# Kernel optimization log

Hardware: AMD Instinct MI355X
Metric: run time of the kernel (lower is better)

The kernel has to match this reference:

```python
import jax, jax.numpy as jnp
import numpy as np


def _causal_conv(x, w, b, dilation):
    # x: (B, Cin, N), w: (Cout, Cin, K) -> causal: left-pad (K-1)*dilation
    pad = (w.shape[-1] - 1) * dilation
    y = jax.lax.conv_general_dilated(
        x, w, window_strides=(1,), padding=[(pad, 0)],
        rhs_dilation=(dilation,), dimension_numbers=('NCH', 'OIH', 'NCH'))
    return y + b[None, :, None]


def setup_inputs() -> dict:
    key = jax.random.key(0)
    ks = jax.random.split(key, 8)
    B, N, C, L = 8, 32768, 16, 30
    s = 0.1  # weight scale to avoid gate saturation
    return {
        'x': jax.random.normal(ks[0], (B, N), dtype=jnp.float32) * 1000.0,  # int16-like samples
        'lengths': jax.random.randint(ks[1], (B,), N // 2, N),
        'w0': jax.random.normal(ks[2], (C, 1, 2), dtype=jnp.float32) * s,
        'b0': jnp.zeros((C,), jnp.float32),
        'wf': jax.random.normal(ks[3], (L - 1, C, C, 2), dtype=jnp.float32) * s,
        'bf': jnp.zeros((L - 1, C), jnp.float32),
        'wg': jax.random.normal(ks[4], (L - 1, C, C, 2), dtype=jnp.float32) * s,
        'bg': jnp.zeros((L - 1, C), jnp.float32),
        'wa': jax.random.normal(ks[5], (64, C), dtype=jnp.float32) * s,
        'ba': jnp.zeros((64,), jnp.float32),
        'wo': jax.random.normal(ks[6], (256, 64), dtype=jnp.float32) * s,
        'bo': jnp.zeros((256,), jnp.float32),
    }


def reference(x, lengths, w0, b0, wf, bf, wg, bg, wa, ba, wo, bo):
    L = wf.shape[0] + 1  # total layers (layer 0 is plain causal conv)
    xin = (x / 32768.0)[:, None, :]            # (B,1,N), int16 normalization 65536/2
    out0 = _causal_conv(xin, w0, b0, 1)        # (B,C,N)
    agg = out0                                 # skip aggregate
    h = xin + out0                             # residual input (broadcast 1->C channels)
    for i in range(1, L):                      # fixed small layer count
        d = 2 ** (i % 10)
        f = _causal_conv(h, wf[i - 1], bf[i - 1], d)
        g = _causal_conv(h, wg[i - 1], bg[i - 1], d)
        out = jnp.tanh(f) * jax.nn.sigmoid(g)  # gated activation unit
        agg = agg + out
        h = h + out
    a = jnp.einsum('oc,bcn->bon', wa, jax.nn.relu(agg)) + ba[None, :, None]  # agregate1x1
    o = jnp.einsum('oc,bcn->bon', wo, jax.nn.relu(a)) + bo[None, :, None]    # output1x1
    o = jax.nn.log_softmax(o, axis=1)
    mask = (jnp.arange(o.shape[-1]) < lengths[:, None]).astype(o.dtype)      # (B,N)
    return o * mask[:, None, :]
```

## Files before the change

### kernel.cpp

```cpp
#include <hip/hip_runtime.h>

#define NSEQ 32768
#define NB 8
#define NC 16
#define LBLK 1024
#define LPX (LBLK / 8)
#define QGRD 4096
#define QPX (QGRD / 8)

typedef float vfloat4 __attribute__((ext_vector_type(4)));

__device__ __forceinline__ float sigm_f(float x) {
    return __fdividef(1.f, 1.f + __expf(-x));
}
__device__ __forceinline__ float tanh_f(float x) {
    return __fdividef(2.f, 1.f + __expf(-2.f * x)) - 1.f;
}

__device__ __forceinline__ void nt_store4(float* p, float a, float b, float c, float d) {
    vfloat4 v; v.x = a; v.y = b; v.z = c; v.w = d;
    __builtin_nontemporal_store(v, (vfloat4*)p);
}

__global__ __launch_bounds__(256) void k_layer0(
    const float* __restrict__ x, const float* __restrict__ w0,
    const float* __restrict__ b0, float* __restrict__ h)
{
    int bid = blockIdx.x;
    int tid = ((bid & 7) * LPX + (bid >> 3)) * 256 + threadIdx.x;
    int n = tid & (NSEQ - 1);
    const float inv = 1.f / 32768.f;
    float xc = x[tid] * inv;
    float xp = (n >= 1) ? x[tid - 1] * inv : 0.f;
    float v[NC];
#pragma unroll
    for (int c = 0; c < NC; c++) {
        float o = w0[c * 2] * xp + w0[c * 2 + 1] * xc + b0[c];
        v[c] = xc + o;
    }
    float* ph = h + (size_t)tid * NC;
#pragma unroll
    for (int i = 0; i < 4; i++)
        nt_store4(ph + i * 4, v[i * 4], v[i * 4 + 1], v[i * 4 + 2], v[i * 4 + 3]);
}

__global__ __launch_bounds__(256, 6) void k_layer(
    const float* __restrict__ hin, float* __restrict__ hout,
    const float* __restrict__ wf, const float* __restrict__ bf,
    const float* __restrict__ wg, const float* __restrict__ bg, int d)
{
    int bid = blockIdx.x;
    int lbid = (bid & 7) * QPX + (bid >> 3);
    int t = threadIdx.x;
    int pos = lbid * 64 + (t & 63);
    int q = __builtin_amdgcn_readfirstlane(t >> 6);
    int n = pos & (NSEQ - 1);

    float hc[NC], hp[NC];
    {
        const float4* pc = (const float4*)(hin + (size_t)pos * NC);
#pragma unroll
        for (int i = 0; i < 4; i++) {
            float4 tv = pc[i];
            hc[i * 4] = tv.x; hc[i * 4 + 1] = tv.y; hc[i * 4 + 2] = tv.z; hc[i * 4 + 3] = tv.w;
        }
    }
    if (n >= d) {
        const float4* pp = (const float4*)(hin + (size_t)(pos - d) * NC);
#pragma unroll
        for (int i = 0; i < 4; i++) {
            float4 tv = pp[i];
            hp[i * 4] = tv.x; hp[i * 4 + 1] = tv.y; hp[i * 4 + 2] = tv.z; hp[i * 4 + 3] = tv.w;
        }
    } else {
#pragma unroll
        for (int i = 0; i < NC; i++) hp[i] = 0.f;
    }

    const int c0 = q * 4;
    float f[4], g[4];
#pragma unroll
    for (int j = 0; j < 4; j++) { f[j] = bf[c0 + j]; g[j] = bg[c0 + j]; }

#pragma unroll
    for (int ci = 0; ci < NC; ci++) {
        float xp = hp[ci], xc = hc[ci];
#pragma unroll
        for (int j = 0; j < 4; j++) {
            int co = c0 + j;
            f[j] = fmaf(wf[(co * NC + ci) * 2 + 0], xp, f[j]);
            f[j] = fmaf(wf[(co * NC + ci) * 2 + 1], xc, f[j]);
            g[j] = fmaf(wg[(co * NC + ci) * 2 + 0], xp, g[j]);
            g[j] = fmaf(wg[(co * NC + ci) * 2 + 1], xc, g[j]);
        }
    }

    float v[4];
#pragma unroll
    for (int j = 0; j < 4; j++) {
        float outv = tanh_f(f[j]) * sigm_f(g[j]);
        v[j] = hc[c0 + j] + outv;
    }
    nt_store4(hout + (size_t)pos * NC + c0, v[0], v[1], v[2], v[3]);
}

__global__ __launch_bounds__(256) void k_prep_t(
    const float* __restrict__ wo, float* __restrict__ woT)
{
    int t = blockIdx.x * 256 + threadIdx.x;
    int k = t >> 6;
    int j = t & 63;
    woT[j * 256 + k] = wo[k * 64 + j];
}

__global__ __launch_bounds__(512, 4) void k_final(
    const float* __restrict__ hfin, const float* __restrict__ x,
    const int* __restrict__ lengths,
    const float* __restrict__ wa, const float* __restrict__ ba,
    const float* __restrict__ woT, const float* __restrict__ bo,
    float* __restrict__ out)
{
    __shared__ float s_r[64][17];
    __shared__ float s_ra[64][65];
    __shared__ float s_red[2][8][64];

    int t = threadIdx.x;
    int p = t & 63;
    int q = __builtin_amdgcn_readfirstlane(t >> 6);
    int blk = blockIdx.x;
    int b = blk >> 9;
    int n0 = (blk & 511) << 6;
    int n = n0 + p;
    size_t pos = (size_t)b * NSEQ + n;
    float xin = x[pos] * (1.f / 32768.f);

    if (q < 4) {
        const float4* ph = (const float4*)(hfin + pos * NC);
        float4 v = ph[q];
        s_r[p][q * 4 + 0] = fmaxf(v.x - xin, 0.f);
        s_r[p][q * 4 + 1] = fmaxf(v.y - xin, 0.f);
        s_r[p][q * 4 + 2] = fmaxf(v.z - xin, 0.f);
        s_r[p][q * 4 + 3] = fmaxf(v.w - xin, 0.f);
    }
    __syncthreads();

    {
        float r[NC];
#pragma unroll
        for (int c = 0; c < NC; c++) r[c] = s_r[p][c];
#pragma unroll
        for (int jj = 0; jj < 8; jj++) {
            int j = q * 8 + jj;
            float acc = ba[j];
#pragma unroll
            for (int c = 0; c < NC; c++) acc = fmaf(wa[j * NC + c], r[c], acc);
            s_ra[p][j] = fmaxf(acc, 0.f);
        }
    }
    __syncthreads();

    float o[32];
#pragma unroll
    for (int kk = 0; kk < 32; kk++) o[kk] = bo[q * 32 + kk];

#pragma unroll 8
    for (int j = 0; j < 64; j++) {
        float rj = s_ra[p][j];
        const float* wcol = woT + j * 256 + q * 32;
#pragma unroll
        for (int kk = 0; kk < 32; kk++)
            o[kk] = fmaf(wcol[kk], rj, o[kk]);
    }

    float m = -1e30f;
#pragma unroll
    for (int kk = 0; kk < 32; kk++) m = fmaxf(m, o[kk]);
    s_red[0][q][p] = m;
    __syncthreads();
    m = fmaxf(fmaxf(fmaxf(s_red[0][0][p], s_red[0][1][p]),
                    fmaxf(s_red[0][2][p], s_red[0][3][p])),
              fmaxf(fmaxf(s_red[0][4][p], s_red[0][5][p]),
                    fmaxf(s_red[0][6][p], s_red[0][7][p])));
    float s = 0.f;
#pragma unroll
    for (int kk = 0; kk < 32; kk++) s += __expf(o[kk] - m);
    s_red[1][q][p] = s;
    __syncthreads();
    s = ((s_red[1][0][p] + s_red[1][1][p]) + (s_red[1][2][p] + s_red[1][3][p]))
      + ((s_red[1][4][p] + s_red[1][5][p]) + (s_red[1][6][p] + s_red[1][7][p]));
    float lse = m + __logf(s);

    bool valid = n < lengths[b];
    float* po = out + ((size_t)b * 256 + q * 32) * NSEQ + n;
#pragma unroll
    for (int kk = 0; kk < 32; kk++) {
        float v = valid ? (o[kk] - lse) : 0.f;
        __builtin_nontemporal_store(v, &po[(size_t)kk * NSEQ]);
    }
}

extern "C" void kernel_launch(void* const* d_in, const int* in_sizes, int n_in,
                              void* d_out, int out_size, void* d_ws, size_t ws_size,
                              hipStream_t stream) {
    const float* x   = (const float*)d_in[0];
    const int* lens  = (const int*)d_in[1];
    const float* w0  = (const float*)d_in[2];
    const float* b0  = (const float*)d_in[3];
    const float* wf  = (const float*)d_in[4];
    const float* bf  = (const float*)d_in[5];
    const float* wg  = (const float*)d_in[6];
    const float* bg  = (const float*)d_in[7];
    const float* wa  = (const float*)d_in[8];
    const float* ba  = (const float*)d_in[9];
    const float* wo  = (const float*)d_in[10];
    const float* bo  = (const float*)d_in[11];
    float* out = (float*)d_out;

    float* hA = (float*)d_ws;
    float* hB = hA + (size_t)NB * NSEQ * NC;
    float* woT = hB + (size_t)NB * NSEQ * NC;

    k_prep_t<<<dim3(64), dim3(256), 0, stream>>>(wo, woT);
    k_layer0<<<dim3(LBLK), dim3(256), 0, stream>>>(x, w0, b0, hA);

    float* cur = hA;
    float* nxt = hB;
    for (int i = 1; i <= 29; i++) {
        int d = 1 << (i % 10);
        k_layer<<<dim3(QGRD), dim3(256), 0, stream>>>(cur, nxt,
                                         wf + (size_t)(i - 1) * NC * NC * 2,
                                         bf + (size_t)(i - 1) * NC,
                                         wg + (size_t)(i - 1) * NC * NC * 2,
                                         bg + (size_t)(i - 1) * NC, d);
        float* tmp = cur; cur = nxt; nxt = tmp;
    }

    dim3 fgrd(NB * (NSEQ / 64));
    k_final<<<fgrd, dim3(512), 0, stream>>>(cur, x, lens, wa, ba, woT, bo, out);
}
```

Baseline: 577.6 us.

## Fuse pairs of small-dilation layers into one kernel with LDS halo

Adds a k_pair kernel that computes two consecutive gated conv layers in one launch. The first layer's output for the 64-position tile, plus a halo of dB earlier positions, is recomputed and kept in shared memory, and the second layer then reads from it. Pairs are used where the second dilation is at most 16 (layers 1-4, 9-14, 19-24), so eight intermediate full-tensor writes and reads to global memory are removed. The cost is redundant computation of halo positions, an extra barrier, and lower occupancy from the shared-memory buffer and launch bounds.

```diff
diff --git a/kernel.cpp b/kernel.cpp
--- a/kernel.cpp
+++ b/kernel.cpp
@@ -102,6 +102,118 @@
         v[j] = hc[c0 + j] + outv;
     }
     nt_store4(hout + (size_t)pos * NC + c0, v[0], v[1], v[2], v[3]);
+}
+
+__global__ __launch_bounds__(256, 5) void k_pair(
+    const float* __restrict__ hin, float* __restrict__ hout,
+    const float* __restrict__ wfA, const float* __restrict__ bfA,
+    const float* __restrict__ wgA, const float* __restrict__ bgA, int dA,
+    const float* __restrict__ wfB, const float* __restrict__ bfB,
+    const float* __restrict__ wgB, const float* __restrict__ bgB, int dB)
+{
+    __shared__ float hsA[NC][80];
+    int bid = blockIdx.x;
+    int lbid = (bid & 7) * QPX + (bid >> 3);
+    int t = threadIdx.x;
+    int lane = t & 63;
+    int q = __builtin_amdgcn_readfirstlane(t >> 6);
+    const int c0 = q * 4;
+    int P = lbid * 64;
+    int n0 = P & (NSEQ - 1);
+
+#pragma unroll 1
+    for (int pass = 0; pass < 2; ++pass) {
+        int pos  = pass ? (P + lane) : (P - dB + lane);
+        int act  = pass ? 1 : ((lane < dB) && (n0 > 0));
+        int slot = pass ? (dB + lane) : lane;
+        if (act) {
+            int n = pos & (NSEQ - 1);
+            float hc[NC], hp[NC];
+            {
+                const float4* pc = (const float4*)(hin + (size_t)pos * NC);
+#pragma unroll
+                for (int i = 0; i < 4; i++) {
+                    float4 tv = pc[i];
+                    hc[i * 4] = tv.x; hc[i * 4 + 1] = tv.y; hc[i * 4 + 2] = tv.z; hc[i * 4 + 3] = tv.w;
+                }
+            }
+            if (n >= dA) {
+                const float4* pp = (const float4*)(hin + (size_t)(pos - dA) * NC);
+#pragma unroll
+                for (int i = 0; i < 4; i++) {
+                    float4 tv = pp[i];
+                    hp[i * 4] = tv.x; hp[i * 4 + 1] = tv.y; hp[i * 4 + 2] = tv.z; hp[i * 4 + 3] = tv.w;
+                }
+            } else {
+#pragma unroll
+                for (int i = 0; i < NC; i++) hp[i] = 0.f;
+            }
+
+            float f[4], g[4];
+#pragma unroll
+            for (int j = 0; j < 4; j++) { f[j] = bfA[c0 + j]; g[j] = bgA[c0 + j]; }
+
+#pragma unroll
+            for (int ci = 0; ci < NC; ci++) {
+                float xp = hp[ci], xc = hc[ci];
+#pragma unroll
+                for (int j = 0; j < 4; j++) {
+                    int co = c0 + j;
+                    f[j] = fmaf(wfA[(co * NC + ci) * 2 + 0], xp, f[j]);
+                    f[j] = fmaf(wfA[(co * NC + ci) * 2 + 1], xc, f[j]);
+                    g[j] = fmaf(wgA[(co * NC + ci) * 2 + 0], xp, g[j]);
+                    g[j] = fmaf(wgA[(co * NC + ci) * 2 + 1], xc, g[j]);
+                }
+            }
+
+#pragma unroll
+            for (int j = 0; j < 4; j++) {
+                float outv = tanh_f(f[j]) * sigm_f(g[j]);
+                hsA[c0 + j][slot] = hc[c0 + j] + outv;
+            }
+        }
+    }
+    __syncthreads();
+
+    {
+        int pos = P + lane;
+        int n = pos & (NSEQ - 1);
+        float hc[NC], hp[NC];
+#pragma unroll
+        for (int c = 0; c < NC; c++) hc[c] = hsA[c][dB + lane];
+        if (n >= dB) {
+#pragma unroll
+            for (int c = 0; c < NC; c++) hp[c] = hsA[c][lane];
+        } else {
+#pragma unroll
+            for (int c = 0; c < NC; c++) hp[c] = 0.f;
+        }
+
+        float f[4], g[4];
+#pragma unroll
+        for (int j = 0; j < 4; j++) { f[j] = bfB[c0 + j]; g[j] = bgB[c0 + j]; }
+
+#pragma unroll
+        for (int ci = 0; ci < NC; ci++) {
+            float xp = hp[ci], xc = hc[ci];
+#pragma unroll
+            for (int j = 0; j < 4; j++) {
+                int co = c0 + j;
+                f[j] = fmaf(wfB[(co * NC + ci) * 2 + 0], xp, f[j]);
+                f[j] = fmaf(wfB[(co * NC + ci) * 2 + 1], xc, f[j]);
+                g[j] = fmaf(wgB[(co * NC + ci) * 2 + 0], xp, g[j]);
+                g[j] = fmaf(wgB[(co * NC + ci) * 2 + 1], xc, g[j]);
+            }
+        }
+
+        float v[4];
+#pragma unroll
+        for (int j = 0; j < 4; j++) {
+            float outv = tanh_f(f[j]) * sigm_f(g[j]);
+            v[j] = hc[c0 + j] + outv;
+        }
+        nt_store4(hout + (size_t)pos * NC + c0, v[0], v[1], v[2], v[3]);
+    }
 }
 
 __global__ __launch_bounds__(256) void k_prep_t(
@@ -220,20 +332,50 @@
     float* hB = hA + (size_t)NB * NSEQ * NC;
     float* woT = hB + (size_t)NB * NSEQ * NC;
 
+    auto WF = [&](int i) { return wf + (size_t)(i - 1) * NC * NC * 2; };
+    auto BF = [&](int i) { return bf + (size_t)(i - 1) * NC; };
+    auto WG = [&](int i) { return wg + (size_t)(i - 1) * NC * NC * 2; };
+    auto BG = [&](int i) { return bg + (size_t)(i - 1) * NC; };
+    auto D  = [&](int i) { return 1 << (i % 10); };
+
     k_prep_t<<<dim3(64), dim3(256), 0, stream>>>(wo, woT);
     k_layer0<<<dim3(LBLK), dim3(256), 0, stream>>>(x, w0, b0, hA);
 
     float* cur = hA;
     float* nxt = hB;
-    for (int i = 1; i <= 29; i++) {
-        int d = 1 << (i % 10);
+    auto single = [&](int i) {
         k_layer<<<dim3(QGRD), dim3(256), 0, stream>>>(cur, nxt,
-                                         wf + (size_t)(i - 1) * NC * NC * 2,
-                                         bf + (size_t)(i - 1) * NC,
-                                         wg + (size_t)(i - 1) * NC * NC * 2,
-                                         bg + (size_t)(i - 1) * NC, d);
+            WF(i), BF(i), WG(i), BG(i), D(i));
         float* tmp = cur; cur = nxt; nxt = tmp;
-    }
+    };
+    auto pair = [&](int iA, int iB) {
+        k_pair<<<dim3(QGRD), dim3(256), 0, stream>>>(cur, nxt,
+            WF(iA), BF(iA), WG(iA), BG(iA), D(iA),
+            WF(iB), BF(iB), WG(iB), BG(iB), D(iB));
+        float* tmp = cur; cur = nxt; nxt = tmp;
+    };
+
+    pair(1, 2);
+    pair(3, 4);
+    single(5);
+    single(6);
+    single(7);
+    single(8);
+    pair(9, 10);
+    pair(11, 12);
+    pair(13, 14);
+    single(15);
+    single(16);
+    single(17);
+    single(18);
+    pair(19, 20);
+    pair(21, 22);
+    pair(23, 24);
+    single(25);
+    single(26);
+    single(27);
+    single(28);
+    single(29);
 
     dim3 fgrd(NB * (NSEQ / 64));
     k_final<<<fgrd, dim3(512), 0, stream>>>(cur, x, lens, wa, ba, woT, bo, out);
```

Result: slower. 709.8 us (+22.9%).
